# Performance work log

Measured on AMD Instinct MI355X. Metric: run time of the kernel, lower is better.

The kernel has to match this reference:

```python
import jax, jax.numpy as jnp
import numpy as np

D_MODEL = 256

def setup_inputs() -> dict:
    key = jax.random.key(0)
    k_x, k_wqkv, k_bqkv, k_wp, k_bp = jax.random.split(key, 5)
    B, T, d = 4, 4096, D_MODEL
    bound_qkv = 1.0 / np.sqrt(d)
    return {
        "x": jax.random.normal(k_x, (B, T, d), dtype=jnp.float32),
        "W_qkv": jax.random.uniform(k_wqkv, (d, 3 * d), jnp.float32, -bound_qkv, bound_qkv),
        "b_qkv": jax.random.uniform(k_bqkv, (3 * d,), jnp.float32, -bound_qkv, bound_qkv),
        "W_proj": jax.random.uniform(k_wp, (d, d), jnp.float32, -bound_qkv, bound_qkv),
        "b_proj": jax.random.uniform(k_bp, (d,), jnp.float32, -bound_qkv, bound_qkv),
    }

def reference(x, W_qkv, b_qkv, W_proj, b_proj):
    B, T, d = x.shape
    qkv = x @ W_qkv + b_qkv                       # (B, T, 3d)
    q, k, v = jnp.split(qkv, 3, axis=-1)          # each (B, T, d)
    scale = 1.0 / np.sqrt(d).astype(np.float32)
    scores = jnp.einsum('btd,bsd->bts', q, k) * scale   # (B, T, T)
    causal = jnp.tril(jnp.ones((T, T), dtype=bool))     # allowed positions
    scores = jnp.where(causal, scores, -jnp.inf)
    weights = jax.nn.softmax(scores, axis=-1)           # (B, T, T)
    ctx = jnp.einsum('bts,bsd->btd', weights, v)        # (B, T, d)
    return ctx @ W_proj + b_proj
```

## Files before the change

kernel.cpp:

```cpp
#include <hip/hip_runtime.h>
#include <math.h>

#define TT 4096
#define BB 4
#define DM 256
#define NSEG_B 144

typedef __attribute__((ext_vector_type(8))) short short8;
typedef __attribute__((ext_vector_type(4))) short short4v;
typedef __attribute__((ext_vector_type(4))) float f32x4;

#define MFMA16(a, b, c) __builtin_amdgcn_mfma_f32_16x16x32_bf16(a, b, c, 0, 0, 0)

#define GL2LDS(gp, lp) __builtin_amdgcn_global_load_lds( \
    (const __attribute__((address_space(1))) unsigned int*)(gp), \
    (__attribute__((address_space(3))) unsigned int*)(lp), 16, 0, 0)

__device__ __forceinline__ short f2b(float f) {
    union { float f; unsigned u; } v; v.f = f;
    unsigned r = v.u + 0x7FFFu + ((v.u >> 16) & 1u);
    return (short)(r >> 16);
}
__device__ __forceinline__ float b2f(short h) {
    union { unsigned u; float f; } v;
    v.u = ((unsigned)(unsigned short)h) << 16;
    return v.f;
}

__global__ __launch_bounds__(256) void transpose_cast2(
    const float* __restrict__ W1, short* __restrict__ Wt1,
    const float* __restrict__ W2, short* __restrict__ Wt2)
{
    __shared__ float T[64 * 68];
    const int tid = threadIdx.x;
    const int by = blockIdx.y;
    const float* W; short* Wt; int N, n0;
    if (by < 12) { W = W1; Wt = Wt1; N = 768; n0 = by * 64; }
    else         { W = W2; Wt = Wt2; N = 256; n0 = (by - 12) * 64; }
    const int k0 = blockIdx.x * 64;
#pragma unroll
    for (int it = 0; it < 4; ++it) {
        int idx = tid + it * 256;
        int r = idx >> 4, c4 = idx & 15;
        *(float4*)&T[r * 68 + c4 * 4] =
            *(const float4*)&W[(size_t)(k0 + r) * N + n0 + c4 * 4];
    }
    __syncthreads();
#pragma unroll
    for (int it = 0; it < 4; ++it) {
        int idx = tid + it * 256;
        int n = idx >> 4, c4 = idx & 15;
        short4v t;
#pragma unroll
        for (int j = 0; j < 4; ++j) t[j] = f2b(T[(c4 * 4 + j) * 68 + n]);
        *(short4v*)&Wt[(size_t)(n0 + n) * 256 + k0 + c4 * 4] = t;
    }
}

__global__ __launch_bounds__(256) void qkv_gemm(
    const float* __restrict__ x, const short* __restrict__ Bt,
    const float* __restrict__ bias, short* __restrict__ qkvb,
    short* __restrict__ VtG)
{
    __shared__ short As[16384];
    __shared__ short Bs[16384];
    __shared__ short Ts[64 * 72];

    const int tid = threadIdx.x;
    const int w = tid >> 6, lane = tid & 63;
    const int l15 = lane & 15, quad = lane >> 4;
    const int m0 = blockIdx.x * 64;
    const int nsup = blockIdx.y * 384;

#pragma unroll
    for (int it = 0; it < 8; ++it) {
        int idx = tid + it * 256;
        int row = ((idx >> 9) << 4) + (idx & 15);
        int col = ((idx >> 6) & 7) * 32 + ((idx >> 4) & 3) * 8;
        const float* src = &x[(size_t)(m0 + row) * 256 + col];
        float4 u = *(const float4*)src, u2 = *(const float4*)(src + 4);
        short8 t;
        t[0] = f2b(u.x);  t[1] = f2b(u.y);  t[2] = f2b(u.z);  t[3] = f2b(u.w);
        t[4] = f2b(u2.x); t[5] = f2b(u2.y); t[6] = f2b(u2.z); t[7] = f2b(u2.w);
        *(short8*)&As[idx * 8] = t;
    }

    for (int t6 = 0; t6 < 6; ++t6) {
        const int n0 = nsup + t6 * 64;
#pragma unroll
        for (int it = 0; it < 8; ++it) {
            int idx = tid + it * 256;
            int n = ((idx >> 9) << 4) + (idx & 15);
            int col = ((idx >> 6) & 7) * 32 + ((idx >> 4) & 3) * 8;
            *(short8*)&Bs[idx * 8] = *(const short8*)&Bt[(size_t)(n0 + n) * 256 + col];
        }
        __syncthreads();

        f32x4 acc[4];
#pragma unroll
        for (int t = 0; t < 4; ++t) acc[t] = (f32x4){0.f, 0.f, 0.f, 0.f};
#pragma unroll
        for (int k0 = 0; k0 < 8; ++k0) {
            short8 a = *(const short8*)&As[((w * 8 + k0) * 64 + lane) * 8];
#pragma unroll
            for (int nt = 0; nt < 4; ++nt) {
                short8 bb = *(const short8*)&Bs[((nt * 8 + k0) * 64 + lane) * 8];
                acc[nt] = MFMA16(a, bb, acc[nt]);
            }
        }

        if (n0 < 512) {
#pragma unroll
            for (int nt = 0; nt < 4; ++nt) {
                int n = n0 + nt * 16 + l15;
                float bv = bias[n];
#pragma unroll
                for (int r = 0; r < 4; ++r)
                    qkvb[(size_t)(m0 + w * 16 + quad * 4 + r) * 768 + n]
                        = f2b(acc[nt][r] + bv);
            }
            __syncthreads();
        } else {
#pragma unroll
            for (int nt = 0; nt < 4; ++nt) {
                int n = n0 + nt * 16 + l15;
                float bv = bias[n];
#pragma unroll
                for (int r = 0; r < 4; ++r)
                    Ts[(nt * 16 + l15) * 72 + w * 16 + quad * 4 + r]
                        = f2b(acc[nt][r] + bv);
            }
            __syncthreads();
            const int d  = tid >> 2;
            const int c  = tid & 3;
            short8 v0 = *(const short8*)&Ts[d * 72 + c * 16];
            short8 v1 = *(const short8*)&Ts[d * 72 + c * 16 + 8];
            const int bg = m0 >> 12, key0 = (m0 & 4095) + c * 16;
            short* dst = &VtG[((size_t)bg * 256 + (n0 - 512) + d) * 4096 + key0];
            *(short8*)dst = v0;
            *(short8*)(dst + 8) = v1;
        }
    }
}

__global__ __launch_bounds__(256, 2) void flash_mfma(
    const short* __restrict__ qkv,
    const short* __restrict__ VtG,
    short* __restrict__ Opart,
    float* __restrict__ L)
{
    __shared__ short Ks[2][8192];
    __shared__ short Vs[2][8192];
    __shared__ short Ps[4096];

    const int tid = threadIdx.x;
    const int w = tid >> 6, lane = tid & 63;
    const int l15 = lane & 15, quad = lane >> 4;

    const int b = blockIdx.x & 3;
    const int e = (NSEG_B - 1) - (blockIdx.x >> 2);
    const int lid = b * NSEG_B + e;
    int p5 = 0;
    while (p5 < 7 && e >= 2 * (p5 + 1) * (p5 + 2)) ++p5;
    int off = e - 2 * p5 * (p5 + 1);
    int qt = 4 * p5 + off / (p5 + 1);
    int s  = off - (off / (p5 + 1)) * (p5 + 1);
    const int kb_lo = s * 16;
    const int kb_hi = min(kb_lo + 16, 4 * (qt + 1));
    const int nunits = kb_hi - kb_lo;

    const size_t base = (size_t)b * TT * 768;
    const int row0 = qt * 128;

    short8 aq[2][8];
#pragma unroll
    for (int rs = 0; rs < 2; ++rs) {
        const short* qrow = &qkv[base + (size_t)(row0 + rs * 64 + w * 16 + l15) * 768 + quad * 8];
#pragma unroll
        for (int k0 = 0; k0 < 8; ++k0)
            aq[rs][k0] = *(const short8*)&qrow[k0 * 32];
    }

#pragma unroll
    for (int it = 0; it < 4; ++it) {
        int idx = tid + it * 256;
        int row = ((idx >> 9) << 4) + (idx & 15);
        int col = ((idx >> 6) & 7) * 32 + ((idx >> 4) & 3) * 8;
        GL2LDS(&qkv[base + (size_t)(kb_lo * 32 + row) * 768 + 256 + col], &Ks[0][idx * 8]);
        int d  = ((idx >> 6) << 4) + (idx & 15);
        int kc = ((idx >> 4) & 3) * 8;
        GL2LDS(&VtG[((size_t)b * 256 + d) * 4096 + kb_lo * 32 + kc], &Vs[0][idx * 8]);
    }

    f32x4 o[2][16];
#pragma unroll
    for (int rs = 0; rs < 2; ++rs)
#pragma unroll
        for (int c = 0; c < 16; ++c) o[rs][c] = (f32x4){0.f, 0.f, 0.f, 0.f};
    float l_acc[2][4] = {{0.f, 0.f, 0.f, 0.f}, {0.f, 0.f, 0.f, 0.f}};

    for (int u = 0; u < nunits; ++u) {
        const int p = u & 1;
        const int j0 = (kb_lo + u) * 32;

        __syncthreads();

        if (u + 1 < nunits) {
            const int j0n = j0 + 32;
#pragma unroll
            for (int it = 0; it < 4; ++it) {
                int idx = tid + it * 256;
                int row = ((idx >> 9) << 4) + (idx & 15);
                int col = ((idx >> 6) & 7) * 32 + ((idx >> 4) & 3) * 8;
                GL2LDS(&qkv[base + (size_t)(j0n + row) * 768 + 256 + col], &Ks[p ^ 1][idx * 8]);
                int d  = ((idx >> 6) << 4) + (idx & 15);
                int kc = ((idx >> 4) & 3) * 8;
                GL2LDS(&VtG[((size_t)b * 256 + d) * 4096 + j0n + kc], &Vs[p ^ 1][idx * 8]);
            }
        }

        f32x4 s4[2][2];
#pragma unroll
        for (int rs = 0; rs < 2; ++rs)
#pragma unroll
            for (int nt = 0; nt < 2; ++nt) s4[rs][nt] = (f32x4){0.f, 0.f, 0.f, 0.f};
#pragma unroll
        for (int k0 = 0; k0 < 8; ++k0) {
#pragma unroll
            for (int nt = 0; nt < 2; ++nt) {
                short8 bb = *(const short8*)&Ks[p][((nt * 8 + k0) * 64 + lane) * 8];
                s4[0][nt] = MFMA16(aq[0][k0], bb, s4[0][nt]);
                s4[1][nt] = MFMA16(aq[1][k0], bb, s4[1][nt]);
            }
        }

#pragma unroll
        for (int rs = 0; rs < 2; ++rs) {
#pragma unroll
            for (int r = 0; r < 4; ++r) {
                const int rg = row0 + rs * 64 + w * 16 + quad * 4 + r;
#pragma unroll
                for (int nt = 0; nt < 2; ++nt) {
                    int jg = j0 + nt * 16 + l15;
                    float xx = s4[rs][nt][r] * 0.0625f;
                    if (jg > rg) xx = -INFINITY;
                    float pv = __expf(fminf(xx, 30.f));
                    l_acc[rs][r] += pv;
                    Ps[((rs * 4 + w) * 64 + (nt * 2 + (l15 >> 3)) * 16 + quad * 4 + r) * 8
                       + (l15 & 7)] = f2b(pv);
                }
            }
        }

        {
            short8 a0 = *(const short8*)&Ps[((0 * 4 + w) * 64 + lane) * 8];
            short8 a1 = *(const short8*)&Ps[((1 * 4 + w) * 64 + lane) * 8];
#pragma unroll
            for (int ct = 0; ct < 16; ++ct) {
                short8 bb = *(const short8*)&Vs[p][(ct * 64 + lane) * 8];
                o[0][ct] = MFMA16(a0, bb, o[0][ct]);
                o[1][ct] = MFMA16(a1, bb, o[1][ct]);
            }
        }
    }

#pragma unroll
    for (int rs = 0; rs < 2; ++rs)
#pragma unroll
        for (int r = 0; r < 4; ++r) {
            float l = l_acc[rs][r];
            l += __shfl_xor(l, 1); l += __shfl_xor(l, 2);
            l += __shfl_xor(l, 4); l += __shfl_xor(l, 8);
            if (l15 == 0)
                L[(size_t)lid * 128 + rs * 64 + w * 16 + quad * 4 + r] = l;
        }
    const size_t ob = (size_t)lid * (128 * 256);
#pragma unroll
    for (int rs = 0; rs < 2; ++rs)
#pragma unroll
        for (int r = 0; r < 4; ++r) {
            int lr = rs * 64 + w * 16 + quad * 4 + r;
#pragma unroll
            for (int c = 0; c < 16; ++c)
                Opart[ob + (size_t)lr * 256 + c * 16 + l15] = f2b(o[rs][c][r]);
        }
}

__global__ __launch_bounds__(256) void proj_gemm(
    const short* __restrict__ Opart, const float* __restrict__ L,
    const short* __restrict__ Bt, const float* __restrict__ bias,
    float* __restrict__ out)
{
    __shared__ short As[16384];
    __shared__ short Bs[16384];
    __shared__ float Linv[64];

    const int tid = threadIdx.x;
    const int w = tid >> 6, lane = tid & 63;
    const int l15 = lane & 15, quad = lane >> 4;
    const int t = blockIdx.x;
    const int b = t >> 6, q64 = t & 63;
    const int qt = q64 >> 1, half = q64 & 1;
    const int p5 = qt >> 2;
    const int sbase = b * NSEG_B + 2 * p5 * (p5 + 1) + (qt & 3) * (p5 + 1);
    const int nseg = p5 + 1;
    const int m0 = t * 64;
    const int ro = half * 64;

    if (tid < 64) {
        float l = 0.f;
#pragma unroll
        for (int s2 = 0; s2 < 8; ++s2)
            if (s2 < nseg) l += L[(size_t)(sbase + s2) * 128 + ro + tid];
        Linv[tid] = 1.f / l;
    }
    __syncthreads();

#pragma unroll
    for (int it = 0; it < 8; ++it) {
        int idx = tid + it * 256;
        int row = ((idx >> 9) << 4) + (idx & 15);
        int col = ((idx >> 6) & 7) * 32 + ((idx >> 4) & 3) * 8;
        float a8[8] = {0.f, 0.f, 0.f, 0.f, 0.f, 0.f, 0.f, 0.f};
#pragma unroll
        for (int s2 = 0; s2 < 8; ++s2) {
            if (s2 < nseg) {
                short8 v = *(const short8*)&Opart[(size_t)(sbase + s2) * 32768
                                                  + (size_t)(ro + row) * 256 + col];
#pragma unroll
                for (int j = 0; j < 8; ++j) a8[j] += b2f(v[j]);
            }
        }
        float inv = Linv[row];
        short8 t8;
#pragma unroll
        for (int j = 0; j < 8; ++j) t8[j] = f2b(a8[j] * inv);
        *(short8*)&As[idx * 8] = t8;
    }

    for (int t2 = 0; t2 < 2; ++t2) {
        const int n0 = blockIdx.y * 128 + t2 * 64;
#pragma unroll
        for (int it = 0; it < 8; ++it) {
            int idx = tid + it * 256;
            int n = ((idx >> 9) << 4) + (idx & 15);
            int col = ((idx >> 6) & 7) * 32 + ((idx >> 4) & 3) * 8;
            *(short8*)&Bs[idx * 8] = *(const short8*)&Bt[(size_t)(n0 + n) * 256 + col];
        }
        __syncthreads();

        f32x4 acc[4];
#pragma unroll
        for (int tt = 0; tt < 4; ++tt) acc[tt] = (f32x4){0.f, 0.f, 0.f, 0.f};
#pragma unroll
        for (int k0 = 0; k0 < 8; ++k0) {
            short8 a = *(const short8*)&As[((w * 8 + k0) * 64 + lane) * 8];
#pragma unroll
            for (int nt = 0; nt < 4; ++nt) {
                short8 bb = *(const short8*)&Bs[((nt * 8 + k0) * 64 + lane) * 8];
                acc[nt] = MFMA16(a, bb, acc[nt]);
            }
        }
#pragma unroll
        for (int nt = 0; nt < 4; ++nt) {
            int n = n0 + nt * 16 + l15;
            float bv = bias[n];
#pragma unroll
            for (int r = 0; r < 4; ++r)
                out[(size_t)(m0 + w * 16 + quad * 4 + r) * 256 + n] = acc[nt][r] + bv;
        }
        __syncthreads();
    }
}

extern "C" void kernel_launch(void* const* d_in, const int* in_sizes, int n_in,
                              void* d_out, int out_size, void* d_ws, size_t ws_size,
                              hipStream_t stream)
{
    const float* x     = (const float*)d_in[0];
    const float* Wqkv  = (const float*)d_in[1];
    const float* bqkv  = (const float*)d_in[2];
    const float* Wproj = (const float*)d_in[3];
    const float* bproj = (const float*)d_in[4];
    float* out = (float*)d_out;

    const size_t M = (size_t)BB * TT;
    short* qkv_b  = (short*)d_ws;
    short* Wt1    = qkv_b + M * 768;
    short* Wt2    = Wt1 + (size_t)768 * 256;
    short* VtG    = Wt2 + (size_t)256 * 256;
    short* OpartB = VtG + (size_t)BB * 256 * 4096;
    float* L      = (float*)(OpartB + (size_t)4 * NSEG_B * 128 * 256);

    dim3 blk(256);
    transpose_cast2<<<dim3(4, 16), blk, 0, stream>>>(Wqkv, Wt1, Wproj, Wt2);
    qkv_gemm<<<dim3(256, 2), blk, 0, stream>>>(x, Wt1, bqkv, qkv_b, VtG);
    flash_mfma<<<dim3(BB * NSEG_B), blk, 0, stream>>>(qkv_b, VtG, OpartB, L);
    proj_gemm<<<dim3(256, 2), blk, 0, stream>>>(OpartB, L, Wt2, bproj, out);
}
```

Before: 227.6 us.

## Enlarge flash query tile to 256 rows with 512-thread blocks and rebalance split-K segments

Flash attention blocks now cover 256 query rows with 8 waves, sharing each K/V tile across twice as many queries. Key ranges are split into 12-tile segments, giving a new per-query-tile segment count. The Q/K buffer drops the unused V columns, shrinking its stride from 768 to 512. The projection kernel now runs one block per 64 rows and loops over all four output column tiles instead of using a second grid dimension. The goal is less redundant K/V loading and fewer partial outputs to reduce, at the cost of fewer, larger blocks and possibly lower occupancy and worse tail balance.

```diff
diff --git a/kernel.cpp b/kernel.cpp
--- a/kernel.cpp
+++ b/kernel.cpp
@@ -4,7 +4,7 @@
 #define TT 4096
 #define BB 4
 #define DM 256
-#define NSEG_B 144
+#define NSEG_B 96
 
 typedef __attribute__((ext_vector_type(8))) short short8;
 typedef __attribute__((ext_vector_type(4))) short short4v;
@@ -59,7 +59,7 @@
 
 __global__ __launch_bounds__(256) void qkv_gemm(
     const float* __restrict__ x, const short* __restrict__ Bt,
-    const float* __restrict__ bias, short* __restrict__ qkvb,
+    const float* __restrict__ bias, short* __restrict__ qkb,
     short* __restrict__ VtG)
 {
     __shared__ short As[16384];
@@ -116,7 +116,7 @@
                 float bv = bias[n];
 #pragma unroll
                 for (int r = 0; r < 4; ++r)
-                    qkvb[(size_t)(m0 + w * 16 + quad * 4 + r) * 768 + n]
+                    qkb[(size_t)(m0 + w * 16 + quad * 4 + r) * 512 + n]
                         = f2b(acc[nt][r] + bv);
             }
             __syncthreads();
@@ -143,15 +143,15 @@
     }
 }
 
-__global__ __launch_bounds__(256, 2) void flash_mfma(
-    const short* __restrict__ qkv,
+__global__ __launch_bounds__(512, 2) void flash_mfma(
+    const short* __restrict__ qkb,
     const short* __restrict__ VtG,
     short* __restrict__ Opart,
     float* __restrict__ L)
 {
     __shared__ short Ks[2][8192];
     __shared__ short Vs[2][8192];
-    __shared__ short Ps[4096];
+    __shared__ short Ps[8192];
 
     const int tid = threadIdx.x;
     const int w = tid >> 6, lane = tid & 63;
@@ -160,33 +160,35 @@
     const int b = blockIdx.x & 3;
     const int e = (NSEG_B - 1) - (blockIdx.x >> 2);
     const int lid = b * NSEG_B + e;
-    int p5 = 0;
-    while (p5 < 7 && e >= 2 * (p5 + 1) * (p5 + 2)) ++p5;
-    int off = e - 2 * p5 * (p5 + 1);
-    int qt = 4 * p5 + off / (p5 + 1);
-    int s  = off - (off / (p5 + 1)) * (p5 + 1);
-    const int kb_lo = s * 16;
-    const int kb_hi = min(kb_lo + 16, 4 * (qt + 1));
+    int qt = 0, c = 0;
+    while (qt < 15) {
+        int ns = (2 * (qt + 1) + 2) / 3;
+        if (e < c + ns) break;
+        c += ns; ++qt;
+    }
+    const int s = e - c;
+    const int kb_lo = s * 12;
+    const int kb_hi = min(kb_lo + 12, 8 * (qt + 1));
     const int nunits = kb_hi - kb_lo;
 
-    const size_t base = (size_t)b * TT * 768;
-    const int row0 = qt * 128;
+    const size_t qbase = (size_t)b * TT * 512;
+    const int row0 = qt * 256;
 
     short8 aq[2][8];
 #pragma unroll
     for (int rs = 0; rs < 2; ++rs) {
-        const short* qrow = &qkv[base + (size_t)(row0 + rs * 64 + w * 16 + l15) * 768 + quad * 8];
+        const short* qrow = &qkb[qbase + (size_t)(row0 + rs * 128 + w * 16 + l15) * 512 + quad * 8];
 #pragma unroll
         for (int k0 = 0; k0 < 8; ++k0)
             aq[rs][k0] = *(const short8*)&qrow[k0 * 32];
     }
 
 #pragma unroll
-    for (int it = 0; it < 4; ++it) {
-        int idx = tid + it * 256;
+    for (int it = 0; it < 2; ++it) {
+        int idx = tid + it * 512;
         int row = ((idx >> 9) << 4) + (idx & 15);
         int col = ((idx >> 6) & 7) * 32 + ((idx >> 4) & 3) * 8;
-        GL2LDS(&qkv[base + (size_t)(kb_lo * 32 + row) * 768 + 256 + col], &Ks[0][idx * 8]);
+        GL2LDS(&qkb[qbase + (size_t)(kb_lo * 32 + row) * 512 + 256 + col], &Ks[0][idx * 8]);
         int d  = ((idx >> 6) << 4) + (idx & 15);
         int kc = ((idx >> 4) & 3) * 8;
         GL2LDS(&VtG[((size_t)b * 256 + d) * 4096 + kb_lo * 32 + kc], &Vs[0][idx * 8]);
@@ -196,7 +198,7 @@
 #pragma unroll
     for (int rs = 0; rs < 2; ++rs)
 #pragma unroll
-        for (int c = 0; c < 16; ++c) o[rs][c] = (f32x4){0.f, 0.f, 0.f, 0.f};
+        for (int c2 = 0; c2 < 16; ++c2) o[rs][c2] = (f32x4){0.f, 0.f, 0.f, 0.f};
     float l_acc[2][4] = {{0.f, 0.f, 0.f, 0.f}, {0.f, 0.f, 0.f, 0.f}};
 
     for (int u = 0; u < nunits; ++u) {
@@ -208,11 +210,11 @@
         if (u + 1 < nunits) {
             const int j0n = j0 + 32;
 #pragma unroll
-            for (int it = 0; it < 4; ++it) {
-                int idx = tid + it * 256;
+            for (int it = 0; it < 2; ++it) {
+                int idx = tid + it * 512;
                 int row = ((idx >> 9) << 4) + (idx & 15);
                 int col = ((idx >> 6) & 7) * 32 + ((idx >> 4) & 3) * 8;
-                GL2LDS(&qkv[base + (size_t)(j0n + row) * 768 + 256 + col], &Ks[p ^ 1][idx * 8]);
+                GL2LDS(&qkb[qbase + (size_t)(j0n + row) * 512 + 256 + col], &Ks[p ^ 1][idx * 8]);
                 int d  = ((idx >> 6) << 4) + (idx & 15);
                 int kc = ((idx >> 4) & 3) * 8;
                 GL2LDS(&VtG[((size_t)b * 256 + d) * 4096 + j0n + kc], &Vs[p ^ 1][idx * 8]);
@@ -238,7 +240,7 @@
         for (int rs = 0; rs < 2; ++rs) {
 #pragma unroll
             for (int r = 0; r < 4; ++r) {
-                const int rg = row0 + rs * 64 + w * 16 + quad * 4 + r;
+                const int rg = row0 + rs * 128 + w * 16 + quad * 4 + r;
 #pragma unroll
                 for (int nt = 0; nt < 2; ++nt) {
                     int jg = j0 + nt * 16 + l15;
@@ -246,15 +248,15 @@
                     if (jg > rg) xx = -INFINITY;
                     float pv = __expf(fminf(xx, 30.f));
                     l_acc[rs][r] += pv;
-                    Ps[((rs * 4 + w) * 64 + (nt * 2 + (l15 >> 3)) * 16 + quad * 4 + r) * 8
+                    Ps[((rs * 8 + w) * 64 + (nt * 2 + (l15 >> 3)) * 16 + quad * 4 + r) * 8
                        + (l15 & 7)] = f2b(pv);
                 }
             }
         }
 
         {
-            short8 a0 = *(const short8*)&Ps[((0 * 4 + w) * 64 + lane) * 8];
-            short8 a1 = *(const short8*)&Ps[((1 * 4 + w) * 64 + lane) * 8];
+            short8 a0 = *(const short8*)&Ps[((0 * 8 + w) * 64 + lane) * 8];
+            short8 a1 = *(const short8*)&Ps[((1 * 8 + w) * 64 + lane) * 8];
 #pragma unroll
             for (int ct = 0; ct < 16; ++ct) {
                 short8 bb = *(const short8*)&Vs[p][(ct * 64 + lane) * 8];
@@ -272,17 +274,17 @@
             l += __shfl_xor(l, 1); l += __shfl_xor(l, 2);
             l += __shfl_xor(l, 4); l += __shfl_xor(l, 8);
             if (l15 == 0)
-                L[(size_t)lid * 128 + rs * 64 + w * 16 + quad * 4 + r] = l;
-        }
-    const size_t ob = (size_t)lid * (128 * 256);
+                L[(size_t)lid * 256 + rs * 128 + w * 16 + quad * 4 + r] = l;
+        }
+    const size_t ob = (size_t)lid * (256 * 256);
 #pragma unroll
     for (int rs = 0; rs < 2; ++rs)
 #pragma unroll
         for (int r = 0; r < 4; ++r) {
-            int lr = rs * 64 + w * 16 + quad * 4 + r;
-#pragma unroll
-            for (int c = 0; c < 16; ++c)
-                Opart[ob + (size_t)lr * 256 + c * 16 + l15] = f2b(o[rs][c][r]);
+            int lr = rs * 128 + w * 16 + quad * 4 + r;
+#pragma unroll
+            for (int c2 = 0; c2 < 16; ++c2)
+                Opart[ob + (size_t)lr * 256 + c2 * 16 + l15] = f2b(o[rs][c2][r]);
         }
 }
 
@@ -300,18 +302,18 @@
     const int l15 = lane & 15, quad = lane >> 4;
     const int t = blockIdx.x;
     const int b = t >> 6, q64 = t & 63;
-    const int qt = q64 >> 1, half = q64 & 1;
-    const int p5 = qt >> 2;
-    const int sbase = b * NSEG_B + 2 * p5 * (p5 + 1) + (qt & 3) * (p5 + 1);
-    const int nseg = p5 + 1;
+    const int qt = q64 >> 2;
+    const int quarter = q64 & 3;
+    int sbase = b * NSEG_B;
+    for (int q = 0; q < qt; ++q) sbase += (2 * (q + 1) + 2) / 3;
+    const int nseg = (2 * (qt + 1) + 2) / 3;
     const int m0 = t * 64;
-    const int ro = half * 64;
+    const int ro = quarter * 64;
 
     if (tid < 64) {
         float l = 0.f;
-#pragma unroll
-        for (int s2 = 0; s2 < 8; ++s2)
-            if (s2 < nseg) l += L[(size_t)(sbase + s2) * 128 + ro + tid];
+        for (int s2 = 0; s2 < nseg; ++s2)
+            l += L[(size_t)(sbase + s2) * 256 + ro + tid];
         Linv[tid] = 1.f / l;
     }
     __syncthreads();
@@ -322,14 +324,11 @@
         int row = ((idx >> 9) << 4) + (idx & 15);
         int col = ((idx >> 6) & 7) * 32 + ((idx >> 4) & 3) * 8;
         float a8[8] = {0.f, 0.f, 0.f, 0.f, 0.f, 0.f, 0.f, 0.f};
-#pragma unroll
-        for (int s2 = 0; s2 < 8; ++s2) {
-            if (s2 < nseg) {
-                short8 v = *(const short8*)&Opart[(size_t)(sbase + s2) * 32768
-                                                  + (size_t)(ro + row) * 256 + col];
-#pragma unroll
-                for (int j = 0; j < 8; ++j) a8[j] += b2f(v[j]);
-            }
+        for (int s2 = 0; s2 < nseg; ++s2) {
+            short8 v = *(const short8*)&Opart[(size_t)(sbase + s2) * 65536
+                                              + (size_t)(ro + row) * 256 + col];
+#pragma unroll
+            for (int j = 0; j < 8; ++j) a8[j] += b2f(v[j]);
         }
         float inv = Linv[row];
         short8 t8;
@@ -338,8 +337,8 @@
         *(short8*)&As[idx * 8] = t8;
     }
 
-    for (int t2 = 0; t2 < 2; ++t2) {
-        const int n0 = blockIdx.y * 128 + t2 * 64;
+    for (int t2 = 0; t2 < 4; ++t2) {
+        const int n0 = t2 * 64;
 #pragma unroll
         for (int it = 0; it < 8; ++it) {
             int idx = tid + it * 256;
@@ -385,16 +384,16 @@
     float* out = (float*)d_out;
 
     const size_t M = (size_t)BB * TT;
-    short* qkv_b  = (short*)d_ws;
-    short* Wt1    = qkv_b + M * 768;
+    short* qk_b   = (short*)d_ws;
+    short* Wt1    = qk_b + M * 512;
     short* Wt2    = Wt1 + (size_t)768 * 256;
     short* VtG    = Wt2 + (size_t)256 * 256;
     short* OpartB = VtG + (size_t)BB * 256 * 4096;
-    float* L      = (float*)(OpartB + (size_t)4 * NSEG_B * 128 * 256);
+    float* L      = (float*)(OpartB + (size_t)4 * NSEG_B * 256 * 256);
 
     dim3 blk(256);
     transpose_cast2<<<dim3(4, 16), blk, 0, stream>>>(Wqkv, Wt1, Wproj, Wt2);
-    qkv_gemm<<<dim3(256, 2), blk, 0, stream>>>(x, Wt1, bqkv, qkv_b, VtG);
-    flash_mfma<<<dim3(BB * NSEG_B), blk, 0, stream>>>(qkv_b, VtG, OpartB, L);
-    proj_gemm<<<dim3(256, 2), blk, 0, stream>>>(OpartB, L, Wt2, bproj, out);
-}
+    qkv_gemm<<<dim3(256, 2), blk, 0, stream>>>(x, Wt1, bqkv, qk_b, VtG);
+    flash_mfma<<<dim3(BB * NSEG_B), dim3(512), 0, stream>>>(qk_b, VtG, OpartB, L);
+    proj_gemm<<<dim3(256), blk, 0, stream>>>(OpartB, L, Wt2, bproj, out);
+}
```

New measurement: 221.3 us. -2.8%, faster.
